# Optimization experiments

Hardware: AMD Instinct MI355X
Metric: run time of the kernel (lower is better)

The kernel has to match this reference:

```python
import jax, jax.numpy as jnp
import numpy as np

N_NODES = 50000
N_EDGES = 800000
NUM_GRAPHS = 512
IN_DIM = 128
HID = 128
OUT_DIM = 1


def setup_inputs() -> dict:
    key = jax.random.key(0)
    ks = jax.random.split(key, 8)
    x = jax.random.normal(ks[0], (N_NODES, IN_DIM), dtype=jnp.float32)
    edge_index = jax.random.randint(ks[1], (2, N_EDGES), 0, N_NODES, dtype=jnp.int64)
    batch = jnp.sort(jax.random.randint(ks[2], (N_NODES,), 0, NUM_GRAPHS, dtype=jnp.int64))
    s1 = 1.0 / np.sqrt(IN_DIM)
    s2 = 1.0 / np.sqrt(HID)
    W1 = jax.random.normal(ks[3], (IN_DIM, HID), dtype=jnp.float32) * s1
    b1 = jnp.zeros((HID,), dtype=jnp.float32)
    W2 = jax.random.normal(ks[4], (HID, HID), dtype=jnp.float32) * s2
    b2 = jnp.zeros((HID,), dtype=jnp.float32)
    Wl = jax.random.normal(ks[5], (HID, OUT_DIM), dtype=jnp.float32) * s2
    bl = jnp.zeros((OUT_DIM,), dtype=jnp.float32)
    return {"x": x, "edge_index": edge_index, "batch": batch,
            "W1": W1, "b1": b1, "W2": W2, "b2": b2, "Wl": Wl, "bl": bl}


def _gcn_conv(x, src, dst, norm, W, b):
    # GCNConv: D^{-1/2}(A+I)D^{-1/2} X W + b (self-loops already in src/dst)
    h = x @ W                                    # [N, H]
    msg = h[src] * norm[:, None]                 # gather + edge-normalize
    agg = jax.ops.segment_sum(msg, dst, num_segments=N_NODES)  # scatter-add
    return agg + b


def reference(x, edge_index, batch, W1, b1, W2, b2, Wl, bl):
    loops = jnp.arange(N_NODES, dtype=edge_index.dtype)
    src = jnp.concatenate([edge_index[0], loops])
    dst = jnp.concatenate([edge_index[1], loops])
    deg = jax.ops.segment_sum(jnp.ones_like(dst, dtype=x.dtype), dst, num_segments=N_NODES)
    dinv = jax.lax.rsqrt(deg)                    # deg >= 1 due to self-loops
    norm = dinv[src] * dinv[dst]                 # symmetric normalization per edge

    h = jax.nn.relu(_gcn_conv(x, src, dst, norm, W1, b1))
    h = jax.nn.relu(_gcn_conv(h, src, dst, norm, W2, b2))

    # global_mean_pool over graph ids
    sums = jax.ops.segment_sum(h, batch, num_segments=NUM_GRAPHS)
    cnts = jax.ops.segment_sum(jnp.ones((N_NODES,), dtype=h.dtype), batch, num_segments=NUM_GRAPHS)
    pooled = sums / jnp.maximum(cnts, 1.0)[:, None]

    out = jax.nn.sigmoid(pooled @ Wl + bl)       # [G, 1]
    return out.squeeze(1)                        # [G]
```

## Files before the change

kernel.cpp:

```cpp
#include <hip/hip_runtime.h>
#include <hip/hip_bf16.h>

#define N_NODES 50000
#define N_EDGES 800000
#define NUM_GRAPHS 512
#define MAXDEG 64
#define EPB 4096
#define P1_BLOCKS 196
#define NBUCK 256
#define NPB 196

typedef short short8 __attribute__((ext_vector_type(8)));
typedef unsigned short u16x8 __attribute__((ext_vector_type(8)));
typedef float f32x4 __attribute__((ext_vector_type(4)));

__device__ __forceinline__ unsigned short f2bu(float f) {
    __hip_bfloat16 h = __float2bfloat16(f);
    return *reinterpret_cast<unsigned short*>(&h);
}
__device__ __forceinline__ float bu2f(unsigned short u) {
    unsigned int v = ((unsigned int)u) << 16;
    float f;
    __builtin_memcpy(&f, &v, 4);
    return f;
}

__global__ __launch_bounds__(256) void bin_k(const int* __restrict__ ei,
                                             unsigned int* __restrict__ staging,
                                             int* __restrict__ cnts_tbl,
                                             int* __restrict__ offs_tbl,
                                             unsigned short* __restrict__ hs1,
                                             unsigned short* __restrict__ hs2) {
    __shared__ unsigned int st[EPB];
    __shared__ int cnt[NBUCK], cur[NBUCK], scan[NBUCK];
    int b = blockIdx.x, t = threadIdx.x;
    if (b == 0 && t < 64)
        ((unsigned int*)(hs1 + (size_t)N_NODES * 128))[t] = 0u;
    if (b == 1 && t < 64)
        ((unsigned int*)(hs2 + (size_t)N_NODES * 128))[t] = 0u;
    cnt[t] = 0;
    __syncthreads();

    int e0 = b * EPB;
    int srcv[16], dstv[16], bk[16];
#pragma unroll
    for (int k = 0; k < 16; ++k) {
        int e = e0 + k * 256 + t;
        bool ok = e < N_EDGES;
        srcv[k] = ok ? ei[e] : 0;
        dstv[k] = ok ? ei[N_EDGES + e] : 0;
        bk[k] = ok ? (dstv[k] / NPB) : -1;
        if (ok) atomicAdd(&cnt[bk[k]], 1);
    }
    __syncthreads();
    scan[t] = cnt[t];
    __syncthreads();
    for (int off = 1; off < 256; off <<= 1) {
        int u = t >= off ? scan[t - off] : 0;
        __syncthreads();
        scan[t] += u;
        __syncthreads();
    }
    int excl = scan[t] - cnt[t];
    cur[t] = excl;
    cnts_tbl[t * P1_BLOCKS + b] = cnt[t];
    offs_tbl[t * P1_BLOCKS + b] = excl;
    __syncthreads();
#pragma unroll
    for (int k = 0; k < 16; ++k) {
        if (bk[k] >= 0) {
            int pos = atomicAdd(&cur[bk[k]], 1);
            int dl = dstv[k] - bk[k] * NPB;
            st[pos] = (unsigned int)srcv[k] | ((unsigned int)dl << 16);
        }
    }
    __syncthreads();
    unsigned int* gout = staging + (size_t)b * EPB;
    for (int i = t; i < EPB; i += 256) gout[i] = st[i];
}

__global__ __launch_bounds__(256) void adjbuild_k(const unsigned int* __restrict__ staging,
                                                  const int* __restrict__ cnts_tbl,
                                                  const int* __restrict__ offs_tbl,
                                                  unsigned short* __restrict__ adj,
                                                  int* __restrict__ cnt,
                                                  float* __restrict__ dinv,
                                                  const float* __restrict__ W1,
                                                  const float* __restrict__ W2,
                                                  unsigned short* __restrict__ W1t,
                                                  unsigned short* __restrict__ W2t) {
    int b = blockIdx.x, t = threadIdx.x;
    if (b >= NBUCK) {
        int wb = b - NBUCK;
        const float* W = wb < 64 ? W1 : W2;
        unsigned short* Wt = wb < 64 ? W1t : W2t;
        int idx = (wb & 63) * 256 + t;
        int k = idx >> 7, n = idx & 127;
        Wt[n * 128 + k] = f2bu(W[idx]);
        return;
    }
    __shared__ unsigned short adjL[NPB * MAXDEG];
    __shared__ int cntL[NPB];
    __shared__ int segStart[P1_BLOCKS + 1];
    __shared__ int segOff[P1_BLOCKS];
    __shared__ int tmp[256];

    if (t < NPB) cntL[t] = 0;
    int c = t < P1_BLOCKS ? cnts_tbl[b * P1_BLOCKS + t] : 0;
    if (t < P1_BLOCKS) segOff[t] = offs_tbl[b * P1_BLOCKS + t];
    tmp[t] = c;
    __syncthreads();
    for (int off = 1; off < 256; off <<= 1) {
        int u = t >= off ? tmp[t - off] : 0;
        __syncthreads();
        tmp[t] += u;
        __syncthreads();
    }
    if (t < P1_BLOCKS) segStart[t] = tmp[t] - c;
    if (t == 0) segStart[P1_BLOCKS] = tmp[P1_BLOCKS - 1];
    __syncthreads();

    int T = segStart[P1_BLOCKS];
    for (int f = t; f < T; f += 256) {
        int lo = 0, hi = P1_BLOCKS;
        while (hi - lo > 1) {
            int m = (lo + hi) >> 1;
            if (segStart[m] <= f) lo = m; else hi = m;
        }
        unsigned int p = staging[(size_t)lo * EPB + segOff[lo] + (f - segStart[lo])];
        int src = p & 0xFFFF;
        int dl = p >> 16;
        int slot = atomicAdd(&cntL[dl], 1);
        if (slot < MAXDEG - 1) adjL[dl * MAXDEG + slot] = (unsigned short)src;
    }
    __syncthreads();

    int nodeBase = b * NPB;
    if (t < NPB) {
        int node = nodeBase + t;
        int cc = cntL[t];
        int ec = cc < MAXDEG - 1 ? cc : MAXDEG - 1;
        adjL[t * MAXDEG + ec] = (unsigned short)node;
        int tot = ec + 1, tot4 = (tot + 3) & ~3;
        for (int s = tot; s < tot4; ++s) adjL[t * MAXDEG + s] = (unsigned short)N_NODES;
        if (node < N_NODES) {
            cnt[node] = cc;
            dinv[node] = rsqrtf((float)cc + 1.0f);
        }
    }
    __syncthreads();
    unsigned int* g = (unsigned int*)(adj + (size_t)nodeBase * MAXDEG);
    const unsigned int* l = (const unsigned int*)adjL;
    for (int i = t; i < NPB * MAXDEG / 2; i += 256) g[i] = l[i];
}

template <bool F32A>
__global__ __launch_bounds__(256) void gemm_k(const void* __restrict__ Ap,
                                              const unsigned short* __restrict__ Wt,
                                              const float* __restrict__ dinv,
                                              unsigned short* __restrict__ C) {
    __shared__ unsigned short Wl[128 * 136];
    int t = threadIdx.x;
    for (int idx = t; idx < 2048; idx += 256) {
        int n = idx >> 4, c = idx & 15;
        *(u16x8*)(Wl + n * 136 + c * 8) = *(const u16x8*)(Wt + n * 128 + c * 8);
    }
    __syncthreads();

    int wave = t >> 6, lane = t & 63, quad = lane >> 4, ln = lane & 15;
    int rb = blockIdx.x * 128 + wave * 16;

    short8 a[2][4];
#pragma unroll
    for (int mt = 0; mt < 2; ++mt) {
        int r = rb + mt * 64 + ln;
        r = r < N_NODES ? r : N_NODES - 1;
        if (F32A) {
            const float* arow = (const float*)Ap + (size_t)r * 128 + quad * 8;
#pragma unroll
            for (int ks = 0; ks < 4; ++ks) {
                float4 v0 = *(const float4*)(arow + ks * 32);
                float4 v1 = *(const float4*)(arow + ks * 32 + 4);
                short8 av;
                av[0] = (short)f2bu(v0.x); av[1] = (short)f2bu(v0.y);
                av[2] = (short)f2bu(v0.z); av[3] = (short)f2bu(v0.w);
                av[4] = (short)f2bu(v1.x); av[5] = (short)f2bu(v1.y);
                av[6] = (short)f2bu(v1.z); av[7] = (short)f2bu(v1.w);
                a[mt][ks] = av;
            }
        } else {
            const unsigned short* arow = (const unsigned short*)Ap + (size_t)r * 128 + quad * 8;
#pragma unroll
            for (int ks = 0; ks < 4; ++ks) a[mt][ks] = *(const short8*)(arow + ks * 32);
        }
    }

    f32x4 acc[2][8];
#pragma unroll
    for (int mt = 0; mt < 2; ++mt)
#pragma unroll
        for (int ct = 0; ct < 8; ++ct) acc[mt][ct] = (f32x4){0.f, 0.f, 0.f, 0.f};

#pragma unroll
    for (int ks = 0; ks < 4; ++ks)
#pragma unroll
        for (int ct = 0; ct < 8; ++ct) {
            short8 b = *(const short8*)(Wl + (ct * 16 + ln) * 136 + ks * 32 + quad * 8);
            acc[0][ct] = __builtin_amdgcn_mfma_f32_16x16x32_bf16(a[0][ks], b, acc[0][ct], 0, 0, 0);
            acc[1][ct] = __builtin_amdgcn_mfma_f32_16x16x32_bf16(a[1][ks], b, acc[1][ct], 0, 0, 0);
        }

#pragma unroll
    for (int mt = 0; mt < 2; ++mt) {
#pragma unroll
        for (int rr = 0; rr < 4; ++rr) {
            int r = rb + mt * 64 + quad * 4 + rr;
            if (r >= N_NODES) continue;
            float dv = dinv[r];
#pragma unroll
            for (int ct = 0; ct < 8; ++ct)
                C[(size_t)r * 128 + ct * 16 + ln] = f2bu(acc[mt][ct][rr] * dv);
        }
    }
}

__global__ __launch_bounds__(256) void agg1_k(const unsigned short* __restrict__ hs,
                                              const unsigned short* __restrict__ adj,
                                              const int* __restrict__ cnt,
                                              const float* __restrict__ dinv,
                                              const float* __restrict__ bias,
                                              unsigned short* __restrict__ out) {
    int wave = threadIdx.x >> 6, lane = threadIdx.x & 63;
    int node0 = blockIdx.x * 8 + wave * 2;
    int node1 = node0 + 1;
    int quad = lane >> 4, fl = lane & 15;
    int idx0 = (int)adj[node0 * MAXDEG + lane];
    int idx1 = (int)adj[node1 * MAXDEG + lane];
    int c0 = cnt[node0], c1 = cnt[node1];
    int ec0 = c0 < MAXDEG - 1 ? c0 : MAXDEG - 1;
    int ec1 = c1 < MAXDEG - 1 ? c1 : MAXDEG - 1;
    int it0 = (ec0 + 4) >> 2;
    int it1 = (ec1 + 4) >> 2;
    int common = it0 < it1 ? it0 : it1;

    float a0[8], a1[8];
#pragma unroll
    for (int j = 0; j < 8; ++j) { a0[j] = 0.f; a1[j] = 0.f; }

    int i = 0;
    for (; i + 2 <= common; i += 2) {
        int sA0 = __shfl(idx0, i * 4 + quad, 64);
        int sA1 = __shfl(idx0, i * 4 + 4 + quad, 64);
        int sB0 = __shfl(idx1, i * 4 + quad, 64);
        int sB1 = __shfl(idx1, i * 4 + 4 + quad, 64);
        u16x8 vA0 = *(const u16x8*)(hs + (size_t)sA0 * 128 + fl * 8);
        u16x8 vA1 = *(const u16x8*)(hs + (size_t)sA1 * 128 + fl * 8);
        u16x8 vB0 = *(const u16x8*)(hs + (size_t)sB0 * 128 + fl * 8);
        u16x8 vB1 = *(const u16x8*)(hs + (size_t)sB1 * 128 + fl * 8);
#pragma unroll
        for (int j = 0; j < 8; ++j) {
            a0[j] += bu2f(vA0[j]) + bu2f(vA1[j]);
            a1[j] += bu2f(vB0[j]) + bu2f(vB1[j]);
        }
    }
    for (; i < common; ++i) {
        int sA = __shfl(idx0, i * 4 + quad, 64);
        int sB = __shfl(idx1, i * 4 + quad, 64);
        u16x8 vA = *(const u16x8*)(hs + (size_t)sA * 128 + fl * 8);
        u16x8 vB = *(const u16x8*)(hs + (size_t)sB * 128 + fl * 8);
#pragma unroll
        for (int j = 0; j < 8; ++j) { a0[j] += bu2f(vA[j]); a1[j] += bu2f(vB[j]); }
    }
    for (; i < it0; ++i) {
        int sA = __shfl(idx0, i * 4 + quad, 64);
        u16x8 vA = *(const u16x8*)(hs + (size_t)sA * 128 + fl * 8);
#pragma unroll
        for (int j = 0; j < 8; ++j) a0[j] += bu2f(vA[j]);
    }
    for (; i < it1; ++i) {
        int sB = __shfl(idx1, i * 4 + quad, 64);
        u16x8 vB = *(const u16x8*)(hs + (size_t)sB * 128 + fl * 8);
#pragma unroll
        for (int j = 0; j < 8; ++j) a1[j] += bu2f(vB[j]);
    }

#pragma unroll
    for (int j = 0; j < 8; ++j) {
        a0[j] += __shfl_xor(a0[j], 16, 64);
        a0[j] += __shfl_xor(a0[j], 32, 64);
        a1[j] += __shfl_xor(a1[j], 16, 64);
        a1[j] += __shfl_xor(a1[j], 32, 64);
    }

    if (quad < 2) {
        int node = quad == 0 ? node0 : node1;
        const float* av = nullptr;
        float dv = dinv[node];
        float4 b0 = *(const float4*)(bias + fl * 8);
        float4 b1 = *(const float4*)(bias + fl * 8 + 4);
        float r0 = quad == 0 ? a0[0] : a1[0];
        float r1 = quad == 0 ? a0[1] : a1[1];
        float r2 = quad == 0 ? a0[2] : a1[2];
        float r3 = quad == 0 ? a0[3] : a1[3];
        float r4 = quad == 0 ? a0[4] : a1[4];
        float r5 = quad == 0 ? a0[5] : a1[5];
        float r6 = quad == 0 ? a0[6] : a1[6];
        float r7 = quad == 0 ? a0[7] : a1[7];
        u16x8 o;
        o[0] = f2bu(fmaxf(r0 * dv + b0.x, 0.f));
        o[1] = f2bu(fmaxf(r1 * dv + b0.y, 0.f));
        o[2] = f2bu(fmaxf(r2 * dv + b0.z, 0.f));
        o[3] = f2bu(fmaxf(r3 * dv + b0.w, 0.f));
        o[4] = f2bu(fmaxf(r4 * dv + b1.x, 0.f));
        o[5] = f2bu(fmaxf(r5 * dv + b1.y, 0.f));
        o[6] = f2bu(fmaxf(r6 * dv + b1.z, 0.f));
        o[7] = f2bu(fmaxf(r7 * dv + b1.w, 0.f));
        *(u16x8*)(out + (size_t)node * 128 + fl * 8) = o;
        (void)av;
    }
}

__global__ __launch_bounds__(256) void agg_dot_k(const unsigned short* __restrict__ hs,
                                                 const unsigned short* __restrict__ adj,
                                                 const int* __restrict__ cnt,
                                                 const float* __restrict__ dinv,
                                                 const float* __restrict__ bias,
                                                 const float* __restrict__ Wl,
                                                 float* __restrict__ pnode) {
    int wave = threadIdx.x >> 6, lane = threadIdx.x & 63;
    int node0 = blockIdx.x * 8 + wave * 2;
    int node1 = node0 + 1;
    int quad = lane >> 4, fl = lane & 15;
    int idx0 = (int)adj[node0 * MAXDEG + lane];
    int idx1 = (int)adj[node1 * MAXDEG + lane];
    int c0 = cnt[node0], c1 = cnt[node1];
    int ec0 = c0 < MAXDEG - 1 ? c0 : MAXDEG - 1;
    int ec1 = c1 < MAXDEG - 1 ? c1 : MAXDEG - 1;
    int it0 = (ec0 + 4) >> 2;
    int it1 = (ec1 + 4) >> 2;
    int common = it0 < it1 ? it0 : it1;

    float a0[8], a1[8];
#pragma unroll
    for (int j = 0; j < 8; ++j) { a0[j] = 0.f; a1[j] = 0.f; }

    int i = 0;
    for (; i + 2 <= common; i += 2) {
        int sA0 = __shfl(idx0, i * 4 + quad, 64);
        int sA1 = __shfl(idx0, i * 4 + 4 + quad, 64);
        int sB0 = __shfl(idx1, i * 4 + quad, 64);
        int sB1 = __shfl(idx1, i * 4 + 4 + quad, 64);
        u16x8 vA0 = *(const u16x8*)(hs + (size_t)sA0 * 128 + fl * 8);
        u16x8 vA1 = *(const u16x8*)(hs + (size_t)sA1 * 128 + fl * 8);
        u16x8 vB0 = *(const u16x8*)(hs + (size_t)sB0 * 128 + fl * 8);
        u16x8 vB1 = *(const u16x8*)(hs + (size_t)sB1 * 128 + fl * 8);
#pragma unroll
        for (int j = 0; j < 8; ++j) {
            a0[j] += bu2f(vA0[j]) + bu2f(vA1[j]);
            a1[j] += bu2f(vB0[j]) + bu2f(vB1[j]);
        }
    }
    for (; i < common; ++i) {
        int sA = __shfl(idx0, i * 4 + quad, 64);
        int sB = __shfl(idx1, i * 4 + quad, 64);
        u16x8 vA = *(const u16x8*)(hs + (size_t)sA * 128 + fl * 8);
        u16x8 vB = *(const u16x8*)(hs + (size_t)sB * 128 + fl * 8);
#pragma unroll
        for (int j = 0; j < 8; ++j) { a0[j] += bu2f(vA[j]); a1[j] += bu2f(vB[j]); }
    }
    for (; i < it0; ++i) {
        int sA = __shfl(idx0, i * 4 + quad, 64);
        u16x8 vA = *(const u16x8*)(hs + (size_t)sA * 128 + fl * 8);
#pragma unroll
        for (int j = 0; j < 8; ++j) a0[j] += bu2f(vA[j]);
    }
    for (; i < it1; ++i) {
        int sB = __shfl(idx1, i * 4 + quad, 64);
        u16x8 vB = *(const u16x8*)(hs + (size_t)sB * 128 + fl * 8);
#pragma unroll
        for (int j = 0; j < 8; ++j) a1[j] += bu2f(vB[j]);
    }

#pragma unroll
    for (int j = 0; j < 8; ++j) {
        a0[j] += __shfl_xor(a0[j], 16, 64);
        a0[j] += __shfl_xor(a0[j], 32, 64);
        a1[j] += __shfl_xor(a1[j], 16, 64);
        a1[j] += __shfl_xor(a1[j], 32, 64);
    }

    float dv0 = dinv[node0], dv1 = dinv[node1];
    float4 b0 = *(const float4*)(bias + fl * 8);
    float4 b1 = *(const float4*)(bias + fl * 8 + 4);
    float4 w0 = *(const float4*)(Wl + fl * 8);
    float4 w1 = *(const float4*)(Wl + fl * 8 + 4);
    float p0 = fmaxf(a0[0] * dv0 + b0.x, 0.f) * w0.x
             + fmaxf(a0[1] * dv0 + b0.y, 0.f) * w0.y
             + fmaxf(a0[2] * dv0 + b0.z, 0.f) * w0.z
             + fmaxf(a0[3] * dv0 + b0.w, 0.f) * w0.w
             + fmaxf(a0[4] * dv0 + b1.x, 0.f) * w1.x
             + fmaxf(a0[5] * dv0 + b1.y, 0.f) * w1.y
             + fmaxf(a0[6] * dv0 + b1.z, 0.f) * w1.z
             + fmaxf(a0[7] * dv0 + b1.w, 0.f) * w1.w;
    float p1 = fmaxf(a1[0] * dv1 + b0.x, 0.f) * w0.x
             + fmaxf(a1[1] * dv1 + b0.y, 0.f) * w0.y
             + fmaxf(a1[2] * dv1 + b0.z, 0.f) * w0.z
             + fmaxf(a1[3] * dv1 + b0.w, 0.f) * w0.w
             + fmaxf(a1[4] * dv1 + b1.x, 0.f) * w1.x
             + fmaxf(a1[5] * dv1 + b1.y, 0.f) * w1.y
             + fmaxf(a1[6] * dv1 + b1.z, 0.f) * w1.z
             + fmaxf(a1[7] * dv1 + b1.w, 0.f) * w1.w;
    p0 += __shfl_xor(p0, 1, 64);
    p0 += __shfl_xor(p0, 2, 64);
    p0 += __shfl_xor(p0, 4, 64);
    p0 += __shfl_xor(p0, 8, 64);
    p1 += __shfl_xor(p1, 1, 64);
    p1 += __shfl_xor(p1, 2, 64);
    p1 += __shfl_xor(p1, 4, 64);
    p1 += __shfl_xor(p1, 8, 64);
    if (lane == 0) {
        float2 pw; pw.x = p0; pw.y = p1;
        *(float2*)(pnode + node0) = pw;
    }
}

__device__ __forceinline__ int lb(const int* a, int n, int v) {
    int lo = 0, hi = n;
    while (lo < hi) {
        int m = (lo + hi) >> 1;
        if (a[m] < v) lo = m + 1;
        else hi = m;
    }
    return lo;
}

__global__ __launch_bounds__(64) void final_k(const float* __restrict__ pnode,
                                              const int* __restrict__ batch,
                                              const float* __restrict__ bl,
                                              float* __restrict__ out) {
    int g = blockIdx.x, t = threadIdx.x;
    int lo = lb(batch, N_NODES, g), hi = lb(batch, N_NODES, g + 1);
    float s = 0.f;
    for (int r = lo + t; r < hi; r += 64) s += pnode[r];
#pragma unroll
    for (int o = 32; o > 0; o >>= 1) s += __shfl_down(s, o, 64);
    if (t == 0) {
        float cf = (float)(hi - lo);
        float z = s / fmaxf(cf, 1.f) + bl[0];
        out[g] = 1.f / (1.f + expf(-z));
    }
}

extern "C" void kernel_launch(void* const* d_in, const int* in_sizes, int n_in,
                              void* d_out, int out_size, void* d_ws, size_t ws_size,
                              hipStream_t stream) {
    const float* x = (const float*)d_in[0];
    const int* ei = (const int*)d_in[1];
    const int* batch = (const int*)d_in[2];
    const float* W1 = (const float*)d_in[3];
    const float* b1 = (const float*)d_in[4];
    const float* W2 = (const float*)d_in[5];
    const float* b2 = (const float*)d_in[6];
    const float* Wl = (const float*)d_in[7];
    const float* bl = (const float*)d_in[8];
    float* out = (float*)d_out;

    char* ws = (char*)d_ws;
    unsigned int* staging = (unsigned int*)(ws + 0x0);
    int* cnts_tbl = (int*)(ws + 0x310000);
    int* offs_tbl = (int*)(ws + 0x341000);
    unsigned short* adj = (unsigned short*)(ws + 0x372000);
    int* cnt = (int*)(ws + 0x992000);
    float* dinv = (float*)(ws + 0x9C3000);
    unsigned short* W1t = (unsigned short*)(ws + 0x9F4000);
    unsigned short* W2t = (unsigned short*)(ws + 0x9FC000);
    float* pnode = (float*)(ws + 0xA04000);
    unsigned short* hs1 = (unsigned short*)(ws + 0xA36000);
    unsigned short* h1 = (unsigned short*)(ws + 0x1672000);
    unsigned short* hs2 = (unsigned short*)(ws + 0x22AE000);

    bin_k<<<P1_BLOCKS, 256, 0, stream>>>(ei, staging, cnts_tbl, offs_tbl, hs1, hs2);
    adjbuild_k<<<NBUCK + 128, 256, 0, stream>>>(staging, cnts_tbl, offs_tbl,
                                                adj, cnt, dinv, W1, W2, W1t, W2t);

    gemm_k<true><<<(N_NODES + 127) / 128, 256, 0, stream>>>(x, W1t, dinv, hs1);
    agg1_k<<<N_NODES / 8, 256, 0, stream>>>(hs1, adj, cnt, dinv, b1, h1);
    gemm_k<false><<<(N_NODES + 127) / 128, 256, 0, stream>>>(h1, W2t, dinv, hs2);
    agg_dot_k<<<N_NODES / 8, 256, 0, stream>>>(hs2, adj, cnt, dinv, b2, Wl, pnode);

    final_k<<<NUM_GRAPHS, 64, 0, stream>>>(pnode, batch, bl, out);
}
```

Baseline: 190.6 us.

## Assign one node per 16-lane quad in aggregation kernels, removing cross-quad reductions

The aggregation kernels now map one node to each 16-lane group instead of two nodes per wave with neighbours split across quads. Each quad walks its own padded neighbour list, loading four packed 16-bit indices per shuffle pair and gathering eight rows per unrolled step. This removes the cross-quad shuffle reductions and the idle lanes at output time. The count array now stores the padded length so loop bounds come straight from it. Per-lane work becomes serial over the full degree, which lengthens each thread's dependency chain and can increase divergence between quads.

```diff
diff --git a/kernel.cpp b/kernel.cpp
--- a/kernel.cpp
+++ b/kernel.cpp
@@ -144,7 +144,7 @@
         int tot = ec + 1, tot4 = (tot + 3) & ~3;
         for (int s = tot; s < tot4; ++s) adjL[t * MAXDEG + s] = (unsigned short)N_NODES;
         if (node < N_NODES) {
-            cnt[node] = cc;
+            cnt[node] = tot4;
             dinv[node] = rsqrtf((float)cc + 1.0f);
         }
     }
@@ -230,94 +230,61 @@
                                               const float* __restrict__ dinv,
                                               const float* __restrict__ bias,
                                               unsigned short* __restrict__ out) {
-    int wave = threadIdx.x >> 6, lane = threadIdx.x & 63;
-    int node0 = blockIdx.x * 8 + wave * 2;
-    int node1 = node0 + 1;
-    int quad = lane >> 4, fl = lane & 15;
-    int idx0 = (int)adj[node0 * MAXDEG + lane];
-    int idx1 = (int)adj[node1 * MAXDEG + lane];
-    int c0 = cnt[node0], c1 = cnt[node1];
-    int ec0 = c0 < MAXDEG - 1 ? c0 : MAXDEG - 1;
-    int ec1 = c1 < MAXDEG - 1 ? c1 : MAXDEG - 1;
-    int it0 = (ec0 + 4) >> 2;
-    int it1 = (ec1 + 4) >> 2;
-    int common = it0 < it1 ? it0 : it1;
-
-    float a0[8], a1[8];
-#pragma unroll
-    for (int j = 0; j < 8; ++j) { a0[j] = 0.f; a1[j] = 0.f; }
+    int t = threadIdx.x;
+    int wave = t >> 6, lane = t & 63, quad = lane >> 4, fl = lane & 15;
+    int node = blockIdx.x * 16 + wave * 4 + quad;
+    int2 pack = ((const int2*)(adj + (size_t)node * MAXDEG))[fl];
+    int rounds = cnt[node] >> 2;
+    float dv = dinv[node];
+    float4 b0 = *(const float4*)(bias + fl * 8);
+    float4 b1 = *(const float4*)(bias + fl * 8 + 4);
+    int qb = quad << 4;
+
+    float a[8];
+#pragma unroll
+    for (int j = 0; j < 8; ++j) a[j] = 0.f;
 
     int i = 0;
-    for (; i + 2 <= common; i += 2) {
-        int sA0 = __shfl(idx0, i * 4 + quad, 64);
-        int sA1 = __shfl(idx0, i * 4 + 4 + quad, 64);
-        int sB0 = __shfl(idx1, i * 4 + quad, 64);
-        int sB1 = __shfl(idx1, i * 4 + 4 + quad, 64);
-        u16x8 vA0 = *(const u16x8*)(hs + (size_t)sA0 * 128 + fl * 8);
-        u16x8 vA1 = *(const u16x8*)(hs + (size_t)sA1 * 128 + fl * 8);
-        u16x8 vB0 = *(const u16x8*)(hs + (size_t)sB0 * 128 + fl * 8);
-        u16x8 vB1 = *(const u16x8*)(hs + (size_t)sB1 * 128 + fl * 8);
-#pragma unroll
-        for (int j = 0; j < 8; ++j) {
-            a0[j] += bu2f(vA0[j]) + bu2f(vA1[j]);
-            a1[j] += bu2f(vB0[j]) + bu2f(vB1[j]);
-        }
-    }
-    for (; i < common; ++i) {
-        int sA = __shfl(idx0, i * 4 + quad, 64);
-        int sB = __shfl(idx1, i * 4 + quad, 64);
-        u16x8 vA = *(const u16x8*)(hs + (size_t)sA * 128 + fl * 8);
-        u16x8 vB = *(const u16x8*)(hs + (size_t)sB * 128 + fl * 8);
-#pragma unroll
-        for (int j = 0; j < 8; ++j) { a0[j] += bu2f(vA[j]); a1[j] += bu2f(vB[j]); }
-    }
-    for (; i < it0; ++i) {
-        int sA = __shfl(idx0, i * 4 + quad, 64);
-        u16x8 vA = *(const u16x8*)(hs + (size_t)sA * 128 + fl * 8);
-#pragma unroll
-        for (int j = 0; j < 8; ++j) a0[j] += bu2f(vA[j]);
-    }
-    for (; i < it1; ++i) {
-        int sB = __shfl(idx1, i * 4 + quad, 64);
-        u16x8 vB = *(const u16x8*)(hs + (size_t)sB * 128 + fl * 8);
-#pragma unroll
-        for (int j = 0; j < 8; ++j) a1[j] += bu2f(vB[j]);
-    }
-
-#pragma unroll
-    for (int j = 0; j < 8; ++j) {
-        a0[j] += __shfl_xor(a0[j], 16, 64);
-        a0[j] += __shfl_xor(a0[j], 32, 64);
-        a1[j] += __shfl_xor(a1[j], 16, 64);
-        a1[j] += __shfl_xor(a1[j], 32, 64);
-    }
-
-    if (quad < 2) {
-        int node = quad == 0 ? node0 : node1;
-        const float* av = nullptr;
-        float dv = dinv[node];
-        float4 b0 = *(const float4*)(bias + fl * 8);
-        float4 b1 = *(const float4*)(bias + fl * 8 + 4);
-        float r0 = quad == 0 ? a0[0] : a1[0];
-        float r1 = quad == 0 ? a0[1] : a1[1];
-        float r2 = quad == 0 ? a0[2] : a1[2];
-        float r3 = quad == 0 ? a0[3] : a1[3];
-        float r4 = quad == 0 ? a0[4] : a1[4];
-        float r5 = quad == 0 ? a0[5] : a1[5];
-        float r6 = quad == 0 ? a0[6] : a1[6];
-        float r7 = quad == 0 ? a0[7] : a1[7];
-        u16x8 o;
-        o[0] = f2bu(fmaxf(r0 * dv + b0.x, 0.f));
-        o[1] = f2bu(fmaxf(r1 * dv + b0.y, 0.f));
-        o[2] = f2bu(fmaxf(r2 * dv + b0.z, 0.f));
-        o[3] = f2bu(fmaxf(r3 * dv + b0.w, 0.f));
-        o[4] = f2bu(fmaxf(r4 * dv + b1.x, 0.f));
-        o[5] = f2bu(fmaxf(r5 * dv + b1.y, 0.f));
-        o[6] = f2bu(fmaxf(r6 * dv + b1.z, 0.f));
-        o[7] = f2bu(fmaxf(r7 * dv + b1.w, 0.f));
-        *(u16x8*)(out + (size_t)node * 128 + fl * 8) = o;
-        (void)av;
-    }
+    for (; i + 2 <= rounds; i += 2) {
+        unsigned pAx = (unsigned)__shfl(pack.x, qb + i, 64);
+        unsigned pAy = (unsigned)__shfl(pack.y, qb + i, 64);
+        unsigned pBx = (unsigned)__shfl(pack.x, qb + i + 1, 64);
+        unsigned pBy = (unsigned)__shfl(pack.y, qb + i + 1, 64);
+        u16x8 v0 = *(const u16x8*)(hs + (size_t)(pAx & 0xFFFFu) * 128 + fl * 8);
+        u16x8 v1 = *(const u16x8*)(hs + (size_t)(pAx >> 16) * 128 + fl * 8);
+        u16x8 v2 = *(const u16x8*)(hs + (size_t)(pAy & 0xFFFFu) * 128 + fl * 8);
+        u16x8 v3 = *(const u16x8*)(hs + (size_t)(pAy >> 16) * 128 + fl * 8);
+        u16x8 v4 = *(const u16x8*)(hs + (size_t)(pBx & 0xFFFFu) * 128 + fl * 8);
+        u16x8 v5 = *(const u16x8*)(hs + (size_t)(pBx >> 16) * 128 + fl * 8);
+        u16x8 v6 = *(const u16x8*)(hs + (size_t)(pBy & 0xFFFFu) * 128 + fl * 8);
+        u16x8 v7 = *(const u16x8*)(hs + (size_t)(pBy >> 16) * 128 + fl * 8);
+#pragma unroll
+        for (int j = 0; j < 8; ++j)
+            a[j] += ((bu2f(v0[j]) + bu2f(v1[j])) + (bu2f(v2[j]) + bu2f(v3[j])))
+                  + ((bu2f(v4[j]) + bu2f(v5[j])) + (bu2f(v6[j]) + bu2f(v7[j])));
+    }
+    if (i < rounds) {
+        unsigned px = (unsigned)__shfl(pack.x, qb + i, 64);
+        unsigned py = (unsigned)__shfl(pack.y, qb + i, 64);
+        u16x8 v0 = *(const u16x8*)(hs + (size_t)(px & 0xFFFFu) * 128 + fl * 8);
+        u16x8 v1 = *(const u16x8*)(hs + (size_t)(px >> 16) * 128 + fl * 8);
+        u16x8 v2 = *(const u16x8*)(hs + (size_t)(py & 0xFFFFu) * 128 + fl * 8);
+        u16x8 v3 = *(const u16x8*)(hs + (size_t)(py >> 16) * 128 + fl * 8);
+#pragma unroll
+        for (int j = 0; j < 8; ++j)
+            a[j] += (bu2f(v0[j]) + bu2f(v1[j])) + (bu2f(v2[j]) + bu2f(v3[j]));
+    }
+
+    u16x8 o;
+    o[0] = f2bu(fmaxf(a[0] * dv + b0.x, 0.f));
+    o[1] = f2bu(fmaxf(a[1] * dv + b0.y, 0.f));
+    o[2] = f2bu(fmaxf(a[2] * dv + b0.z, 0.f));
+    o[3] = f2bu(fmaxf(a[3] * dv + b0.w, 0.f));
+    o[4] = f2bu(fmaxf(a[4] * dv + b1.x, 0.f));
+    o[5] = f2bu(fmaxf(a[5] * dv + b1.y, 0.f));
+    o[6] = f2bu(fmaxf(a[6] * dv + b1.z, 0.f));
+    o[7] = f2bu(fmaxf(a[7] * dv + b1.w, 0.f));
+    *(u16x8*)(out + (size_t)node * 128 + fl * 8) = o;
 }
 
 __global__ __launch_bounds__(256) void agg_dot_k(const unsigned short* __restrict__ hs,
@@ -327,101 +294,66 @@
                                                  const float* __restrict__ bias,
                                                  const float* __restrict__ Wl,
                                                  float* __restrict__ pnode) {
-    int wave = threadIdx.x >> 6, lane = threadIdx.x & 63;
-    int node0 = blockIdx.x * 8 + wave * 2;
-    int node1 = node0 + 1;
-    int quad = lane >> 4, fl = lane & 15;
-    int idx0 = (int)adj[node0 * MAXDEG + lane];
-    int idx1 = (int)adj[node1 * MAXDEG + lane];
-    int c0 = cnt[node0], c1 = cnt[node1];
-    int ec0 = c0 < MAXDEG - 1 ? c0 : MAXDEG - 1;
-    int ec1 = c1 < MAXDEG - 1 ? c1 : MAXDEG - 1;
-    int it0 = (ec0 + 4) >> 2;
-    int it1 = (ec1 + 4) >> 2;
-    int common = it0 < it1 ? it0 : it1;
-
-    float a0[8], a1[8];
-#pragma unroll
-    for (int j = 0; j < 8; ++j) { a0[j] = 0.f; a1[j] = 0.f; }
-
-    int i = 0;
-    for (; i + 2 <= common; i += 2) {
-        int sA0 = __shfl(idx0, i * 4 + quad, 64);
-        int sA1 = __shfl(idx0, i * 4 + 4 + quad, 64);
-        int sB0 = __shfl(idx1, i * 4 + quad, 64);
-        int sB1 = __shfl(idx1, i * 4 + 4 + quad, 64);
-        u16x8 vA0 = *(const u16x8*)(hs + (size_t)sA0 * 128 + fl * 8);
-        u16x8 vA1 = *(const u16x8*)(hs + (size_t)sA1 * 128 + fl * 8);
-        u16x8 vB0 = *(const u16x8*)(hs + (size_t)sB0 * 128 + fl * 8);
-        u16x8 vB1 = *(const u16x8*)(hs + (size_t)sB1 * 128 + fl * 8);
-#pragma unroll
-        for (int j = 0; j < 8; ++j) {
-            a0[j] += bu2f(vA0[j]) + bu2f(vA1[j]);
-            a1[j] += bu2f(vB0[j]) + bu2f(vB1[j]);
-        }
-    }
-    for (; i < common; ++i) {
-        int sA = __shfl(idx0, i * 4 + quad, 64);
-        int sB = __shfl(idx1, i * 4 + quad, 64);
-        u16x8 vA = *(const u16x8*)(hs + (size_t)sA * 128 + fl * 8);
-        u16x8 vB = *(const u16x8*)(hs + (size_t)sB * 128 + fl * 8);
-#pragma unroll
-        for (int j = 0; j < 8; ++j) { a0[j] += bu2f(vA[j]); a1[j] += bu2f(vB[j]); }
-    }
-    for (; i < it0; ++i) {
-        int sA = __shfl(idx0, i * 4 + quad, 64);
-        u16x8 vA = *(const u16x8*)(hs + (size_t)sA * 128 + fl * 8);
-#pragma unroll
-        for (int j = 0; j < 8; ++j) a0[j] += bu2f(vA[j]);
-    }
-    for (; i < it1; ++i) {
-        int sB = __shfl(idx1, i * 4 + quad, 64);
-        u16x8 vB = *(const u16x8*)(hs + (size_t)sB * 128 + fl * 8);
-#pragma unroll
-        for (int j = 0; j < 8; ++j) a1[j] += bu2f(vB[j]);
-    }
-
-#pragma unroll
-    for (int j = 0; j < 8; ++j) {
-        a0[j] += __shfl_xor(a0[j], 16, 64);
-        a0[j] += __shfl_xor(a0[j], 32, 64);
-        a1[j] += __shfl_xor(a1[j], 16, 64);
-        a1[j] += __shfl_xor(a1[j], 32, 64);
-    }
-
-    float dv0 = dinv[node0], dv1 = dinv[node1];
+    int t = threadIdx.x;
+    int wave = t >> 6, lane = t & 63, quad = lane >> 4, fl = lane & 15;
+    int node = blockIdx.x * 16 + wave * 4 + quad;
+    int2 pack = ((const int2*)(adj + (size_t)node * MAXDEG))[fl];
+    int rounds = cnt[node] >> 2;
+    float dv = dinv[node];
     float4 b0 = *(const float4*)(bias + fl * 8);
     float4 b1 = *(const float4*)(bias + fl * 8 + 4);
     float4 w0 = *(const float4*)(Wl + fl * 8);
     float4 w1 = *(const float4*)(Wl + fl * 8 + 4);
-    float p0 = fmaxf(a0[0] * dv0 + b0.x, 0.f) * w0.x
-             + fmaxf(a0[1] * dv0 + b0.y, 0.f) * w0.y
-             + fmaxf(a0[2] * dv0 + b0.z, 0.f) * w0.z
-             + fmaxf(a0[3] * dv0 + b0.w, 0.f) * w0.w
-             + fmaxf(a0[4] * dv0 + b1.x, 0.f) * w1.x
-             + fmaxf(a0[5] * dv0 + b1.y, 0.f) * w1.y
-             + fmaxf(a0[6] * dv0 + b1.z, 0.f) * w1.z
-             + fmaxf(a0[7] * dv0 + b1.w, 0.f) * w1.w;
-    float p1 = fmaxf(a1[0] * dv1 + b0.x, 0.f) * w0.x
-             + fmaxf(a1[1] * dv1 + b0.y, 0.f) * w0.y
-             + fmaxf(a1[2] * dv1 + b0.z, 0.f) * w0.z
-             + fmaxf(a1[3] * dv1 + b0.w, 0.f) * w0.w
-             + fmaxf(a1[4] * dv1 + b1.x, 0.f) * w1.x
-             + fmaxf(a1[5] * dv1 + b1.y, 0.f) * w1.y
-             + fmaxf(a1[6] * dv1 + b1.z, 0.f) * w1.z
-             + fmaxf(a1[7] * dv1 + b1.w, 0.f) * w1.w;
-    p0 += __shfl_xor(p0, 1, 64);
-    p0 += __shfl_xor(p0, 2, 64);
-    p0 += __shfl_xor(p0, 4, 64);
-    p0 += __shfl_xor(p0, 8, 64);
-    p1 += __shfl_xor(p1, 1, 64);
-    p1 += __shfl_xor(p1, 2, 64);
-    p1 += __shfl_xor(p1, 4, 64);
-    p1 += __shfl_xor(p1, 8, 64);
-    if (lane == 0) {
-        float2 pw; pw.x = p0; pw.y = p1;
-        *(float2*)(pnode + node0) = pw;
-    }
+    int qb = quad << 4;
+
+    float a[8];
+#pragma unroll
+    for (int j = 0; j < 8; ++j) a[j] = 0.f;
+
+    int i = 0;
+    for (; i + 2 <= rounds; i += 2) {
+        unsigned pAx = (unsigned)__shfl(pack.x, qb + i, 64);
+        unsigned pAy = (unsigned)__shfl(pack.y, qb + i, 64);
+        unsigned pBx = (unsigned)__shfl(pack.x, qb + i + 1, 64);
+        unsigned pBy = (unsigned)__shfl(pack.y, qb + i + 1, 64);
+        u16x8 v0 = *(const u16x8*)(hs + (size_t)(pAx & 0xFFFFu) * 128 + fl * 8);
+        u16x8 v1 = *(const u16x8*)(hs + (size_t)(pAx >> 16) * 128 + fl * 8);
+        u16x8 v2 = *(const u16x8*)(hs + (size_t)(pAy & 0xFFFFu) * 128 + fl * 8);
+        u16x8 v3 = *(const u16x8*)(hs + (size_t)(pAy >> 16) * 128 + fl * 8);
+        u16x8 v4 = *(const u16x8*)(hs + (size_t)(pBx & 0xFFFFu) * 128 + fl * 8);
+        u16x8 v5 = *(const u16x8*)(hs + (size_t)(pBx >> 16) * 128 + fl * 8);
+        u16x8 v6 = *(const u16x8*)(hs + (size_t)(pBy & 0xFFFFu) * 128 + fl * 8);
+        u16x8 v7 = *(const u16x8*)(hs + (size_t)(pBy >> 16) * 128 + fl * 8);
+#pragma unroll
+        for (int j = 0; j < 8; ++j)
+            a[j] += ((bu2f(v0[j]) + bu2f(v1[j])) + (bu2f(v2[j]) + bu2f(v3[j])))
+                  + ((bu2f(v4[j]) + bu2f(v5[j])) + (bu2f(v6[j]) + bu2f(v7[j])));
+    }
+    if (i < rounds) {
+        unsigned px = (unsigned)__shfl(pack.x, qb + i, 64);
+        unsigned py = (unsigned)__shfl(pack.y, qb + i, 64);
+        u16x8 v0 = *(const u16x8*)(hs + (size_t)(px & 0xFFFFu) * 128 + fl * 8);
+        u16x8 v1 = *(const u16x8*)(hs + (size_t)(px >> 16) * 128 + fl * 8);
+        u16x8 v2 = *(const u16x8*)(hs + (size_t)(py & 0xFFFFu) * 128 + fl * 8);
+        u16x8 v3 = *(const u16x8*)(hs + (size_t)(py >> 16) * 128 + fl * 8);
+#pragma unroll
+        for (int j = 0; j < 8; ++j)
+            a[j] += (bu2f(v0[j]) + bu2f(v1[j])) + (bu2f(v2[j]) + bu2f(v3[j]));
+    }
+
+    float p = fmaxf(a[0] * dv + b0.x, 0.f) * w0.x
+            + fmaxf(a[1] * dv + b0.y, 0.f) * w0.y
+            + fmaxf(a[2] * dv + b0.z, 0.f) * w0.z
+            + fmaxf(a[3] * dv + b0.w, 0.f) * w0.w
+            + fmaxf(a[4] * dv + b1.x, 0.f) * w1.x
+            + fmaxf(a[5] * dv + b1.y, 0.f) * w1.y
+            + fmaxf(a[6] * dv + b1.z, 0.f) * w1.z
+            + fmaxf(a[7] * dv + b1.w, 0.f) * w1.w;
+    p += __shfl_xor(p, 1, 64);
+    p += __shfl_xor(p, 2, 64);
+    p += __shfl_xor(p, 4, 64);
+    p += __shfl_xor(p, 8, 64);
+    if (fl == 0) pnode[node] = p;
 }
 
 __device__ __forceinline__ int lb(const int* a, int n, int v) {
@@ -484,9 +416,9 @@
                                                 adj, cnt, dinv, W1, W2, W1t, W2t);
 
     gemm_k<true><<<(N_NODES + 127) / 128, 256, 0, stream>>>(x, W1t, dinv, hs1);
-    agg1_k<<<N_NODES / 8, 256, 0, stream>>>(hs1, adj, cnt, dinv, b1, h1);
+    agg1_k<<<N_NODES / 16, 256, 0, stream>>>(hs1, adj, cnt, dinv, b1, h1);
     gemm_k<false><<<(N_NODES + 127) / 128, 256, 0, stream>>>(h1, W2t, dinv, hs2);
-    agg_dot_k<<<N_NODES / 8, 256, 0, stream>>>(hs2, adj, cnt, dinv, b2, Wl, pnode);
+    agg_dot_k<<<N_NODES / 16, 256, 0, stream>>>(hs2, adj, cnt, dinv, b2, Wl, pnode);
 
     final_k<<<NUM_GRAPHS, 64, 0, stream>>>(pnode, batch, bl, out);
 }
```

After: 190.6 us. Within noise of the previous version (+0.0%).
